# Performance work log

Measured on AMD Instinct MI355X. Metric: run time of the kernel, lower is better.

Reference implementation:

```python
import jax, jax.numpy as jnp
import numpy as np

D_MODEL = 1024
NHEAD = 16
HEAD_DIM = D_MODEL // NHEAD


def setup_inputs() -> dict:
    key = jax.random.key(0)
    ks = jax.random.split(key, 7)
    B, S = 4, 2048
    scale = 1.0 / np.sqrt(D_MODEL)
    x = jax.random.normal(ks[0], (B, S, D_MODEL), dtype=jnp.float32)
    Wq = jax.random.normal(ks[1], (D_MODEL, D_MODEL), dtype=jnp.float32) * scale
    Wk = jax.random.normal(ks[2], (D_MODEL, D_MODEL), dtype=jnp.float32) * scale
    Wv = jax.random.normal(ks[3], (D_MODEL, D_MODEL), dtype=jnp.float32) * scale
    bq = jax.random.normal(ks[4], (D_MODEL,), dtype=jnp.float32) * 0.01
    bk = jax.random.normal(ks[5], (D_MODEL,), dtype=jnp.float32) * 0.01
    bv = jax.random.normal(ks[6], (D_MODEL,), dtype=jnp.float32) * 0.01
    return {"x": x, "Wq": Wq, "bq": bq, "Wk": Wk, "bk": bk, "Wv": Wv, "bv": bv}


def reference(x, Wq, bq, Wk, bk, Wv, bv):
    B, S, _ = x.shape
    # Linear projections (torch Linear: x @ W.T + b; weights here are already [in, out])
    q = x @ Wq + bq
    k = x @ Wk + bk
    v = x @ Wv + bv
    # [B, S, H, Dh] -> [B, H, S, Dh]
    q = q.reshape(B, S, NHEAD, HEAD_DIM).transpose(0, 2, 1, 3)
    k = k.reshape(B, S, NHEAD, HEAD_DIM).transpose(0, 2, 1, 3)
    v = v.reshape(B, S, NHEAD, HEAD_DIM).transpose(0, 2, 1, 3)
    # NOTE: original scales by sqrt(d_model), not sqrt(head_dim)
    scores = jnp.einsum("bhqd,bhkd->bhqk", q, k) / np.sqrt(D_MODEL).astype(np.float32)
    attn = jax.nn.softmax(scores, axis=-1)  # dropout is identity at eval
    out = jnp.einsum("bhqk,bhkd->bhqd", attn, v)
    out = out.transpose(0, 2, 1, 3).reshape(B, S, D_MODEL)
    return out
```

## Files before the change

kernel.cpp:

```cpp
#include <hip/hip_runtime.h>
#include <cstdint>
#include <cstddef>

#define SEQ 2048
#define BATCH 4
#define KVB 64
#define NT (SEQ / KVB)

typedef __attribute__((ext_vector_type(8))) unsigned short u16x8;
typedef __attribute__((ext_vector_type(8))) __bf16 bf16x8;
typedef __attribute__((ext_vector_type(4))) float f32x4;
typedef __attribute__((ext_vector_type(4))) unsigned short u16x4;

#if defined(__has_builtin)
#if __has_builtin(__builtin_amdgcn_exp2f)
#define EXP2(x) __builtin_amdgcn_exp2f(x)
#else
#define EXP2(x) exp2f(x)
#endif
#else
#define EXP2(x) exp2f(x)
#endif

static __device__ __forceinline__ unsigned short f2bf(float f) {
  unsigned u = __builtin_bit_cast(unsigned, f);
  u += 0x7fffu + ((u >> 16) & 1u);
  return (unsigned short)(u >> 16);
}

static __device__ __forceinline__ f32x4 mfma16(u16x8 a, u16x8 b, f32x4 c) {
  return __builtin_amdgcn_mfma_f32_16x16x32_bf16(
      __builtin_bit_cast(bf16x8, a), __builtin_bit_cast(bf16x8, b), c, 0, 0, 0);
}

static __device__ __forceinline__ f32x4 mfma16b(u16x8 a, bf16x8 b, f32x4 c) {
  return __builtin_amdgcn_mfma_f32_16x16x32_bf16(
      __builtin_bit_cast(bf16x8, a), b, c, 0, 0, 0);
}

static __device__ __forceinline__ void gl_lds16(const void* g, void* l) {
  __builtin_amdgcn_global_load_lds(
      (const __attribute__((address_space(1))) void*)g,
      (__attribute__((address_space(3))) void*)l, 16, 0, 0);
}

__global__ __launch_bounds__(256) void k_conv_x(const float* __restrict__ x,
                                                unsigned short* __restrict__ xb) {
  int i = (blockIdx.x * 256 + threadIdx.x) * 8;
  f32x4 a = *reinterpret_cast<const f32x4*>(x + i);
  f32x4 b = *reinterpret_cast<const f32x4*>(x + i + 4);
  u16x8 v;
  v[0] = f2bf(a[0]); v[1] = f2bf(a[1]); v[2] = f2bf(a[2]); v[3] = f2bf(a[3]);
  v[4] = f2bf(b[0]); v[5] = f2bf(b[1]); v[6] = f2bf(b[2]); v[7] = f2bf(b[3]);
  *reinterpret_cast<u16x8*>(xb + i) = v;
}

__global__ __launch_bounds__(256) void k_conv_w(const float* __restrict__ Wq,
                                                const float* __restrict__ Wk,
                                                const float* __restrict__ Wv,
                                                unsigned short* __restrict__ wt) {
  const float* W = (blockIdx.z == 0) ? Wq : (blockIdx.z == 1) ? Wk : Wv;
  unsigned short* dst = wt + (size_t)blockIdx.z * 1024 * 1024;
  __shared__ float tile[32][33];
  int n0 = blockIdx.x * 32, k0 = blockIdx.y * 32;
  int tx = threadIdx.x, ty = threadIdx.y;
#pragma unroll
  for (int i = 0; i < 4; i++) {
    int k = ty + i * 8;
    tile[k][tx] = W[(size_t)(k0 + k) * 1024 + n0 + tx];
  }
  __syncthreads();
#pragma unroll
  for (int i = 0; i < 4; i++) {
    int n = ty + i * 8;
    dst[(size_t)(n0 + n) * 1024 + k0 + tx] = f2bf(tile[tx][n]);
  }
}

__global__ __launch_bounds__(256) void k_qkv_gemm(
    const unsigned short* __restrict__ xb, const unsigned short* __restrict__ wt,
    const float* __restrict__ bq, const float* __restrict__ bk,
    const float* __restrict__ bv,
    unsigned short* __restrict__ qb, unsigned short* __restrict__ kb,
    unsigned short* __restrict__ vt) {
  __shared__ unsigned short Ah[2][128 * 32];
  __shared__ unsigned short Bh[2][128 * 32];
  const int tid = threadIdx.x;
  const int lane = tid & 63, wid = tid >> 6;
  const int ln = lane & 15, g = lane >> 4;
  const int wr = wid >> 1, wc = wid & 1;
  const int dd = blockIdx.x;
  const int xcd = dd & 7, j = dd >> 3;
  const int z = j >> 6, kk = j & 63;
  const int m0 = (((kk >> 3) << 3) | xcd) * 128;
  const int n0 = (kk & 7) * 128;
  const unsigned short* Bt = wt + (size_t)z * 1024 * 1024;

  f32x4 acc[4][4];
#pragma unroll
  for (int i = 0; i < 4; i++)
#pragma unroll
    for (int jj = 0; jj < 4; jj++) acc[i][jj] = f32x4{0.f, 0.f, 0.f, 0.f};

  const int rA0 = tid >> 2, cA0 = tid & 3;
  const int swA = (cA0 ^ ((rA0 >> 1) & 3)) << 3;
  const int rA1 = rA0 + 64;

  const unsigned short* gA0 = xb + (size_t)(m0 + rA0) * 1024 + swA;
  const unsigned short* gA1 = xb + (size_t)(m0 + rA1) * 1024 + swA;
  const unsigned short* gB0 = Bt + (size_t)(n0 + rA0) * 1024 + swA;
  const unsigned short* gB1 = Bt + (size_t)(n0 + rA1) * 1024 + swA;

#define GSTAGE(bb, k0)                                          \
  do {                                                          \
    gl_lds16(gA0 + (k0), &Ah[bb][wid * 512]);                   \
    gl_lds16(gA1 + (k0), &Ah[bb][2048 + wid * 512]);            \
    gl_lds16(gB0 + (k0), &Bh[bb][wid * 512]);                   \
    gl_lds16(gB1 + (k0), &Bh[bb][2048 + wid * 512]);            \
  } while (0)

  const int fsw = (g ^ ((ln >> 1) & 3)) << 3;

  int buf = 0;
  GSTAGE(0, 0);
  __syncthreads();

  for (int k0 = 0; k0 < 1024; k0 += 32) {
    if (k0 + 32 < 1024) GSTAGE(buf ^ 1, k0 + 32);
    u16x8 af[4], bfv[4];
#pragma unroll
    for (int mi = 0; mi < 4; mi++)
      af[mi] = *reinterpret_cast<const u16x8*>(
          &Ah[buf][(wr * 64 + mi * 16 + ln) * 32 + fsw]);
#pragma unroll
    for (int ni = 0; ni < 4; ni++)
      bfv[ni] = *reinterpret_cast<const u16x8*>(
          &Bh[buf][(wc * 64 + ni * 16 + ln) * 32 + fsw]);
#pragma unroll
    for (int mi = 0; mi < 4; mi++)
#pragma unroll
      for (int ni = 0; ni < 4; ni++)
        acc[mi][ni] = mfma16(af[mi], bfv[ni], acc[mi][ni]);
    __syncthreads();
    buf ^= 1;
  }

  const float* bias = (z == 0) ? bq : (z == 1) ? bk : bv;
#pragma unroll
  for (int ni = 0; ni < 4; ni++) {
    int n = n0 + wc * 64 + ni * 16 + ln;
    float bb = bias[n];
    int h = n >> 6, d = n & 63;
#pragma unroll
    for (int mi = 0; mi < 4; mi++) {
      int mb = m0 + wr * 64 + mi * 16 + 4 * g;
      int b = mb >> 11, s = mb & 2047;
      if (z == 2) {
        u16x4 pv;
#pragma unroll
        for (int i = 0; i < 4; i++) pv[i] = f2bf(acc[mi][ni][i] + bb);
        int s4 = s >> 2;
        int u = s4 & 7, blk = s4 >> 3;
        int nu = ((u & 3) << 1) | (u >> 2);
        int sp = ((blk << 3) | nu) << 2;
        *reinterpret_cast<u16x4*>(
            &vt[((size_t)((b * 16 + h) * 64 + d)) * 2048 + sp]) = pv;
      } else {
        unsigned short* dst = (z == 0) ? qb : kb;
        float sc = (z == 0) ? 0.0450842200f : 1.0f;
#pragma unroll
        for (int i = 0; i < 4; i++) {
          dst[((size_t)((b * 16 + h) * 2048) + (s + i)) * 64 + d] =
              f2bf((acc[mi][ni][i] + bb) * sc);
        }
      }
    }
  }
#undef GSTAGE
}

__global__ __launch_bounds__(512) void k_attn(
    const unsigned short* __restrict__ qb, const unsigned short* __restrict__ kb,
    const unsigned short* __restrict__ vt, float* __restrict__ out) {
  __shared__ unsigned short Kl[2][KVB * 64];
  __shared__ unsigned short Vl[2][64 * KVB];
  const int tid = threadIdx.x;
  const int lane = tid & 63, wid = tid >> 6;
  const int ln = lane & 15, g = lane >> 4;
  const int flat = blockIdx.x;
  const int bh = flat & 63, qidx = flat >> 6;
  const int b = bh >> 4, h = bh & 15;
  const int q0 = qidx * 256 + wid * 32;
  const unsigned short* Qp = qb + (size_t)bh * SEQ * 64;
  const unsigned short* Kp = kb + (size_t)bh * SEQ * 64;
  const unsigned short* Vp = vt + (size_t)bh * 64 * SEQ;

  const int kr0 = tid >> 3;
  const int psw = ((tid & 7) ^ (kr0 & 7)) << 3;
  const unsigned short* srcK0 = Kp + (size_t)kr0 * 64 + psw;
  const unsigned short* srcV0 = Vp + (size_t)kr0 * SEQ + psw;

#define STAGE(bb, tt)                                                     \
  do {                                                                    \
    gl_lds16(srcK0 + (size_t)(tt) * (KVB * 64), &Kl[bb][wid * 512]);      \
    gl_lds16(srcV0 + (size_t)(tt) * KVB, &Vl[bb][wid * 512]);             \
  } while (0)

  u16x8 qf[2][2];
#pragma unroll
  for (int qt = 0; qt < 2; qt++)
#pragma unroll
    for (int dc = 0; dc < 2; dc++)
      qf[qt][dc] = *reinterpret_cast<const u16x8*>(
          &Qp[(size_t)(q0 + qt * 16 + ln) * 64 + dc * 32 + g * 8]);

  f32x4 o[4][2];
#pragma unroll
  for (int dt = 0; dt < 4; dt++)
#pragma unroll
    for (int qt = 0; qt < 2; qt++) o[dt][qt] = f32x4{0.f, 0.f, 0.f, 0.f};
  f32x4 lsum[2] = {f32x4{0.f, 0.f, 0.f, 0.f}, f32x4{0.f, 0.f, 0.f, 0.f}};

  u16x8 ones;
#pragma unroll
  for (int i = 0; i < 8; i++) ones[i] = 0x3F80;

  const int lm = ln & 7;
  const int ksw0 = (g ^ lm) << 3;
  const int ksw1 = ((4 + g) ^ lm) << 3;
  const int vsw0 = (g ^ lm) << 3;
  const int vsw1 = ((4 + g) ^ lm) << 3;

  int buf = 0;
  STAGE(0, 0);
  __syncthreads();

  for (int t = 0; t < NT; t++) {
    if (t + 1 < NT) STAGE(buf ^ 1, t + 1);

    const unsigned short* Kb = Kl[buf];
    const unsigned short* Vb = Vl[buf];

    u16x8 kf[4][2];
#pragma unroll
    for (int kt = 0; kt < 4; kt++) {
      int rb = (kt * 16 + ln) * 64;
      kf[kt][0] = *reinterpret_cast<const u16x8*>(&Kb[rb + ksw0]);
      kf[kt][1] = *reinterpret_cast<const u16x8*>(&Kb[rb + ksw1]);
    }

    f32x4 st[2][4];
    __builtin_amdgcn_s_setprio(1);
#pragma unroll
    for (int qt = 0; qt < 2; qt++)
#pragma unroll
      for (int kt = 0; kt < 4; kt++) {
        f32x4 c = f32x4{0.f, 0.f, 0.f, 0.f};
        c = mfma16(kf[kt][0], qf[qt][0], c);
        c = mfma16(kf[kt][1], qf[qt][1], c);
        st[qt][kt] = c;
      }
    __builtin_amdgcn_s_setprio(0);

#pragma unroll
    for (int qt = 0; qt < 2; qt++)
#pragma unroll
      for (int kt = 0; kt < 4; kt++)
#pragma unroll
        for (int i = 0; i < 4; i++)
          st[qt][kt][i] = EXP2(st[qt][kt][i]);

    bf16x8 pb[2][2];
#pragma unroll
    for (int qt = 0; qt < 2; qt++)
#pragma unroll
      for (int ks = 0; ks < 2; ks++)
#pragma unroll
        for (int i = 0; i < 4; i++) {
          pb[qt][ks][i] = (__bf16)st[qt][2 * ks][i];
          pb[qt][ks][4 + i] = (__bf16)st[qt][2 * ks + 1][i];
        }

    __builtin_amdgcn_s_setprio(1);
#pragma unroll
    for (int dt = 0; dt < 4; dt++) {
      int rb = (dt * 16 + ln) * 64;
      u16x8 vf0 = *reinterpret_cast<const u16x8*>(&Vb[rb + vsw0]);
      o[dt][0] = mfma16b(vf0, pb[0][0], o[dt][0]);
      o[dt][1] = mfma16b(vf0, pb[1][0], o[dt][1]);
      u16x8 vf1 = *reinterpret_cast<const u16x8*>(&Vb[rb + vsw1]);
      o[dt][0] = mfma16b(vf1, pb[0][1], o[dt][0]);
      o[dt][1] = mfma16b(vf1, pb[1][1], o[dt][1]);
    }
#pragma unroll
    for (int ks = 0; ks < 2; ks++) {
      lsum[0] = mfma16b(ones, pb[0][ks], lsum[0]);
      lsum[1] = mfma16b(ones, pb[1][ks], lsum[1]);
    }
    __builtin_amdgcn_s_setprio(0);

    __syncthreads();
    buf ^= 1;
  }

  float inv[2] = {1.f / lsum[0][0], 1.f / lsum[1][0]};

#pragma unroll
  for (int qt = 0; qt < 2; qt++) {
    int q = q0 + qt * 16 + ln;
#pragma unroll
    for (int dt = 0; dt < 4; dt++) {
      f32x4 r;
#pragma unroll
      for (int i = 0; i < 4; i++) r[i] = o[dt][qt][i] * inv[qt];
      *reinterpret_cast<f32x4*>(
          &out[((size_t)(b * SEQ + q)) * 1024 + h * 64 + dt * 16 + 4 * g]) = r;
    }
  }
#undef STAGE
}

extern "C" void kernel_launch(void* const* d_in, const int* in_sizes, int n_in,
                              void* d_out, int out_size, void* d_ws, size_t ws_size,
                              hipStream_t stream) {
  (void)in_sizes; (void)n_in; (void)out_size;
  const float* x  = (const float*)d_in[0];
  const float* Wq = (const float*)d_in[1];
  const float* bq = (const float*)d_in[2];
  const float* Wk = (const float*)d_in[3];
  const float* bk = (const float*)d_in[4];
  const float* Wv = (const float*)d_in[5];
  const float* bv = (const float*)d_in[6];
  float* out = (float*)d_out;

  char* ws = (char*)d_ws;
  if (ws_size < 73400320u) return;
  unsigned short* xb    = (unsigned short*)(ws);
  unsigned short* wt    = (unsigned short*)(ws + 16777216);
  unsigned short* qbuf  = (unsigned short*)(ws + 23068672);
  unsigned short* kbuf  = (unsigned short*)(ws + 39845888);
  unsigned short* vtbuf = (unsigned short*)(ws + 56623104);

  k_conv_x<<<4096, 256, 0, stream>>>(x, xb);
  k_conv_w<<<dim3(32, 32, 3), dim3(32, 8), 0, stream>>>(Wq, Wk, Wv, wt);
  k_qkv_gemm<<<dim3(1536), 256, 0, stream>>>(xb, wt, bq, bk, bv,
                                             qbuf, kbuf, vtbuf);
  k_attn<<<dim3(512), dim3(512), 0, stream>>>(qbuf, kbuf, vtbuf, out);
}
```

Before: 152.9 us.

## Triple-buffer QKV GEMM LDS staging with explicit vmcnt waits and MFMA priority

Replaces the double-buffered K loop in the QKV projection GEMM with a three-stage LDS ring. Loads for two tiles ahead stay in flight, guarded by explicit s_waitcnt vmcnt(4) plus raw barriers instead of __syncthreads. It also raises wave priority around the MFMA block. The aim is to hide global-to-LDS latency better, at the cost of 50% more LDS and a dependence on exact vmcnt accounting, which could create races if the async load count assumptions are wrong.

```diff
diff --git a/kernel.cpp b/kernel.cpp
--- a/kernel.cpp
+++ b/kernel.cpp
@@ -83,8 +83,8 @@
     const float* __restrict__ bv,
     unsigned short* __restrict__ qb, unsigned short* __restrict__ kb,
     unsigned short* __restrict__ vt) {
-  __shared__ unsigned short Ah[2][128 * 32];
-  __shared__ unsigned short Bh[2][128 * 32];
+  __shared__ unsigned short Ah[3][128 * 32];
+  __shared__ unsigned short Bh[3][128 * 32];
   const int tid = threadIdx.x;
   const int lane = tid & 63, wid = tid >> 6;
   const int ln = lane & 15, g = lane >> 4;
@@ -121,29 +121,37 @@
 
   const int fsw = (g ^ ((ln >> 1) & 3)) << 3;
 
-  int buf = 0;
+#define GCOMPUTE(bb)                                                       \
+  do {                                                                     \
+    u16x8 af[4], bfv[4];                                                   \
+    _Pragma("unroll") for (int mi = 0; mi < 4; mi++)                       \
+      af[mi] = *reinterpret_cast<const u16x8*>(                            \
+          &Ah[bb][(wr * 64 + mi * 16 + ln) * 32 + fsw]);                   \
+    _Pragma("unroll") for (int ni = 0; ni < 4; ni++)                       \
+      bfv[ni] = *reinterpret_cast<const u16x8*>(                           \
+          &Bh[bb][(wc * 64 + ni * 16 + ln) * 32 + fsw]);                   \
+    __builtin_amdgcn_s_setprio(1);                                         \
+    _Pragma("unroll") for (int mi = 0; mi < 4; mi++)                       \
+    _Pragma("unroll") for (int ni = 0; ni < 4; ni++)                       \
+      acc[mi][ni] = mfma16(af[mi], bfv[ni], acc[mi][ni]);                  \
+    __builtin_amdgcn_s_setprio(0);                                         \
+  } while (0)
+
   GSTAGE(0, 0);
-  __syncthreads();
-
-  for (int k0 = 0; k0 < 1024; k0 += 32) {
-    if (k0 + 32 < 1024) GSTAGE(buf ^ 1, k0 + 32);
-    u16x8 af[4], bfv[4];
-#pragma unroll
-    for (int mi = 0; mi < 4; mi++)
-      af[mi] = *reinterpret_cast<const u16x8*>(
-          &Ah[buf][(wr * 64 + mi * 16 + ln) * 32 + fsw]);
-#pragma unroll
-    for (int ni = 0; ni < 4; ni++)
-      bfv[ni] = *reinterpret_cast<const u16x8*>(
-          &Bh[buf][(wc * 64 + ni * 16 + ln) * 32 + fsw]);
-#pragma unroll
-    for (int mi = 0; mi < 4; mi++)
-#pragma unroll
-      for (int ni = 0; ni < 4; ni++)
-        acc[mi][ni] = mfma16(af[mi], bfv[ni], acc[mi][ni]);
-    __syncthreads();
-    buf ^= 1;
-  }
+  GSTAGE(1, 32);
+  asm volatile("s_waitcnt vmcnt(4)" ::: "memory");
+  __builtin_amdgcn_s_barrier();
+
+  for (int t = 0; t < 30; t++) {
+    GCOMPUTE(t % 3);
+    GSTAGE((t + 2) % 3, (t + 2) * 32);
+    asm volatile("s_waitcnt vmcnt(4)" ::: "memory");
+    __builtin_amdgcn_s_barrier();
+  }
+  GCOMPUTE(0);
+  asm volatile("s_waitcnt vmcnt(0)" ::: "memory");
+  __builtin_amdgcn_s_barrier();
+  GCOMPUTE(1);
 
   const float* bias = (z == 0) ? bq : (z == 1) ? bk : bv;
 #pragma unroll
@@ -177,6 +185,7 @@
     }
   }
 #undef GSTAGE
+#undef GCOMPUTE
 }
 
 __global__ __launch_bounds__(512) void k_attn(
```

Result: no change. 151.6 us (-0.8%).
